# Optimization experiments

Measured on AMD Instinct MI355X. Metric: run time of the kernel, lower is better.

The kernel has to match this reference:

```python
import jax, jax.numpy as jnp
import numpy as np

EPS = 1e-5


def conv2d(x, w, b, pad, mode='reflect'):
    # x: [B,C,H,W], w: [O,I,kh,kw]
    if pad > 0:
        x = jnp.pad(x, ((0, 0), (0, 0), (pad, pad), (pad, pad)), mode=mode)
    y = jax.lax.conv_general_dilated(x, w, (1, 1), 'VALID',
                                     dimension_numbers=('NCHW', 'OIHW', 'NCHW'))
    return y + b[None, :, None, None]


def inorm(x):
    # InstanceNorm2d, no affine (nn.InstanceNorm2d default)
    m = jnp.mean(x, axis=(2, 3), keepdims=True)
    v = jnp.mean((x - m) ** 2, axis=(2, 3), keepdims=True)
    return (x - m) * jax.lax.rsqrt(v + EPS)


def upsample2(x):
    # nn.Upsample(scale_factor=2), default nearest
    return jnp.repeat(jnp.repeat(x, 2, axis=2), 2, axis=3)


def bilinear_sample(img, py, px):
    # img [B,C,H,W]; py/px [B,H,W] float coords; zero padding outside bounds
    B, C, H, W = img.shape
    y0 = jnp.floor(py)
    x0 = jnp.floor(px)
    wy1 = (py - y0)[:, None]
    wx1 = (px - x0)[:, None]
    wy0 = 1.0 - wy1
    wx0 = 1.0 - wx1
    y0i = y0.astype(jnp.int32)
    x0i = x0.astype(jnp.int32)
    flat = img.reshape(B, C, H * W)

    def tap(yi, xi):
        valid = (yi >= 0) & (yi < H) & (xi >= 0) & (xi < W)
        idx = jnp.clip(yi, 0, H - 1) * W + jnp.clip(xi, 0, W - 1)
        g = jnp.take_along_axis(flat, idx.reshape(B, 1, H * W), axis=2).reshape(B, C, H, W)
        return g * valid[:, None]

    return (tap(y0i, x0i) * wy0 * wx0 + tap(y0i, x0i + 1) * wy0 * wx1 +
            tap(y0i + 1, x0i) * wy1 * wx0 + tap(y0i + 1, x0i + 1) * wy1 * wx1)


def mdcn(x, offset, mask, w, b):
    # modulated deformable conv v2: 3x3, stride 1, pad 1, 1 deformable group
    # offset [B,18,H,W] read as interleaved (dy,dx) per kernel tap; mask [B,9,H,W]
    B, C, H, W = x.shape
    off = offset.reshape(B, 9, 2, H, W)
    base_y = jnp.arange(H, dtype=x.dtype)[None, :, None]
    base_x = jnp.arange(W, dtype=x.dtype)[None, None, :]
    cols = []
    for k in range(9):
        ky, kx = k // 3 - 1, k % 3 - 1
        py = base_y + ky + off[:, k, 0]
        px = base_x + kx + off[:, k, 1]
        cols.append(bilinear_sample(x, py, px) * mask[:, k][:, None])
    col = jnp.stack(cols, axis=2)  # [B,C,9,H,W]
    out = jnp.einsum('bckhw,ock->bohw', col, w.reshape(w.shape[0], C, 9))
    return out + b[None, :, None, None]


def dcn_block(out, skip, off_w, off_b, w, b):
    # ModulatedDeformConvPack(double=True): offsets from concat, deform conv on skip
    dc = jnp.concatenate([out, skip], axis=1)
    om = conv2d(dc, off_w, off_b, 1, mode='constant')
    o1, o2, m = jnp.split(om, 3, axis=1)
    offset = jnp.concatenate([o1, o2], axis=1)
    pre = mdcn(skip, offset, jax.nn.sigmoid(m), w, b)
    return jnp.concatenate([pre, out], axis=1), offset


def decoder_fwd(x, skip1, skip2,
                rb0_w1, rb0_b1, rb0_w2, rb0_b2,
                rb1_w1, rb1_b1, rb1_w2, rb1_b2,
                conv1_w, conv1_b, conv3_w, conv3_b,
                conv5_w, conv5_b, conv6_w, conv6_b,
                dcn2_off_w, dcn2_off_b, dcn2_w, dcn2_b,
                dcn1_off_w, dcn1_off_b, dcn1_w, dcn1_b):
    out = x
    # i=0: ResBlocks (2 resblocks, 'in' norm, relu, reflect pad)
    for (w1, b1, w2, b2) in ((rb0_w1, rb0_b1, rb0_w2, rb0_b2),
                             (rb1_w1, rb1_b1, rb1_w2, rb1_b2)):
        h = jax.nn.relu(inorm(conv2d(out, w1, b1, 1)))
        out = out + inorm(conv2d(h, w2, b2, 1))
    # i=1: Conv2dBlock(256->256, 5x5)
    out = jax.nn.relu(inorm(conv2d(out, conv1_w, conv1_b, 2)))
    # dcn_2 hook (baseline_idx=2 -> dcn_idx=[1,3])
    out, offset2 = dcn_block(out, skip2, dcn2_off_w, dcn2_off_b, dcn2_w, dcn2_b)
    # i=2: upsample
    out = upsample2(out)
    # i=3: Conv2dBlock(512->128, 5x5)
    out = jax.nn.relu(inorm(conv2d(out, conv3_w, conv3_b, 2)))
    # dcn hook
    out, offset1 = dcn_block(out, skip1, dcn1_off_w, dcn1_off_b, dcn1_w, dcn1_b)
    # i=4: upsample
    out = upsample2(out)
    # i=5: Conv2dBlock(256->64, 5x5)
    out = jax.nn.relu(inorm(conv2d(out, conv5_w, conv5_b, 2)))
    # i=6: Conv2dBlock(64->3, 7x7, no norm, tanh)
    out = jnp.tanh(conv2d(out, conv6_w, conv6_b, 3))
    offset_sum = 0.5 * (jnp.mean(jnp.abs(offset1)) + jnp.mean(jnp.abs(offset2)))
    return out, offset_sum


def setup_inputs() -> dict:
    key = jax.random.key(0)
    ks = iter(jax.random.split(key, 48))

    def randn(shape, scale=1.0):
        return jax.random.normal(next(ks), shape, dtype=jnp.float32) * scale

    def conv_w(o, i, k, scale=1.0):
        return randn((o, i, k, k), scale / float(np.sqrt(i * k * k)))

    d = {}
    d['x'] = randn((8, 256, 32, 32))
    d['skip1'] = randn((8, 128, 64, 64))
    d['skip2'] = randn((8, 256, 32, 32))
    for r in range(2):
        d[f'rb{r}_w1'] = conv_w(256, 256, 3)
        d[f'rb{r}_b1'] = randn((256,), 0.01)
        d[f'rb{r}_w2'] = conv_w(256, 256, 3)
        d[f'rb{r}_b2'] = randn((256,), 0.01)
    d['conv1_w'] = conv_w(256, 256, 5); d['conv1_b'] = randn((256,), 0.01)
    d['conv3_w'] = conv_w(128, 512, 5); d['conv3_b'] = randn((128,), 0.01)
    d['conv5_w'] = conv_w(64, 256, 5); d['conv5_b'] = randn((64,), 0.01)
    d['conv6_w'] = conv_w(3, 64, 7); d['conv6_b'] = randn((3,), 0.01)
    d['dcn2_off_w'] = conv_w(27, 512, 3, 0.1); d['dcn2_off_b'] = randn((27,), 0.01)
    d['dcn2_w'] = conv_w(256, 256, 3); d['dcn2_b'] = randn((256,), 0.01)
    d['dcn1_off_w'] = conv_w(27, 256, 3, 0.1); d['dcn1_off_b'] = randn((27,), 0.01)
    d['dcn1_w'] = conv_w(128, 128, 3); d['dcn1_b'] = randn((128,), 0.01)
    return d


def reference(x, skip1, skip2,
              rb0_w1, rb0_b1, rb0_w2, rb0_b2,
              rb1_w1, rb1_b1, rb1_w2, rb1_b2,
              conv1_w, conv1_b, conv3_w, conv3_b,
              conv5_w, conv5_b, conv6_w, conv6_b,
              dcn2_off_w, dcn2_off_b, dcn2_w, dcn2_b,
              dcn1_off_w, dcn1_off_b, dcn1_w, dcn1_b):
    return decoder_fwd(x, skip1, skip2,
                       rb0_w1, rb0_b1, rb0_w2, rb0_b2,
                       rb1_w1, rb1_b1, rb1_w2, rb1_b2,
                       conv1_w, conv1_b, conv3_w, conv3_b,
                       conv5_w, conv5_b, conv6_w, conv6_b,
                       dcn2_off_w, dcn2_off_b, dcn2_w, dcn2_b,
                       dcn1_off_w, dcn1_off_b, dcn1_w, dcn1_b)
```

## Files before the change

### kernel.cpp

```cpp
#include <hip/hip_runtime.h>
#include <hip/hip_bf16.h>
#include <math.h>

typedef __hip_bfloat16 bf16;
typedef unsigned short u16;
typedef __attribute__((ext_vector_type(8))) short short8;
typedef __attribute__((ext_vector_type(4))) float f32x4;

__device__ __forceinline__ float LD(const float* p) { return *p; }
__device__ __forceinline__ float LD(const bf16* p)  { return __bfloat162float(*p); }
__device__ __forceinline__ void  ST(float* p, float v) { *p = v; }
__device__ __forceinline__ void  ST(bf16* p, float v)  { *p = __float2bfloat16(v); }
__device__ __forceinline__ u16   f2b(float v) { bf16 h = __float2bfloat16(v); return *reinterpret_cast<u16*>(&h); }
__device__ __forceinline__ float b2fu(u16 u) { bf16 h = *reinterpret_cast<bf16*>(&u); return __bfloat162float(h); }

__global__ __launch_bounds__(256) void copy_kernel(const float* __restrict__ in,
                                                   float* __restrict__ out, int n) {
    int i = blockIdx.x * blockDim.x + threadIdx.x;
    if (i < n) out[i] = in[i];
}

__global__ __launch_bounds__(256) void nhwc_f32_kernel(const float* __restrict__ in,
                                                       float* __restrict__ out,
                                                       int C, int HW)
// ... 119 lines not shown
        int C1, int C,
        const u16* __restrict__ wth, const u16* __restrict__ wtl,
        const float* __restrict__ bias,
        void* __restrict__ outv, int O, int H, int W)
{
    constexpr int KK = K * K;
    constexpr int ATILE = NR * NCOL * 32;
    __shared__ __align__(16) u16 Ah[ATILE];
    __shared__ __align__(16) u16 Al[ASPLIT ? ATILE : 8];

    const int tid  = threadIdx.x;
    const int lane = tid & 63;
    const int wv   = tid >> 6;
    const int ln15 = lane & 15;
    const int quad = lane >> 4;
    const int mi = wv % MW, ni = wv / MW;
    int b, p0;
    if (XPIN) {
        const int flat = blockIdx.x + gridDim.x * blockIdx.y;
        b = flat & 7;
        p0 = (flat >> 3) * (MT * 16 * MW);
    } else {
        b = blockIdx.y;
        p0 = blockIdx.x * (MT * 16 * MW);
    }
    const int obase = blockIdx.z * 64;
    const int HW = H * W;
    const int SH = UP ? (H >> 1) : H;
    const int SW = UP ? (W >> 1) : W;
    const int SHW = SH * SW;
    const int PAD = K / 2;
    const int C2 = C - C1;
    const int nch = C >> 5;

    const int y0 = p0 / W;
    const int rbase = (y0 <= PAD) ? 0 : (UP ? ((y0 - PAD) >> 1) : (y0 - PAD));

    int rs[MT][K], cs[MT][K];
#pragma unroll
    for (int ms = 0; ms < MT; ++ms) {
        const int pm = p0 + mi * (MT * 16) + ms * 16 + ln15;
        const int ym = pm / W, xm = pm - ym * W;
#pragma unroll
        for (int tt = 0; tt < K; ++tt) {
            int yy = ym + tt - PAD;
            yy = yy < 0 ? -yy : yy; yy = yy >= H ? 2 * H - 2 - yy : yy;
            rs[ms][tt] = (UP ? (yy >> 1) : yy) - rbase;
            int xx = xm + tt - PAD;
            xx = xx < 0 ? -xx : xx; xx = xx >= W ? 2 * W - 2 - xx : xx;
            cs[ms][tt] = UP ? (xx >> 1) : xx;
        }
    }

    f32x4 acc[MT][2];
#pragma unroll
    for (int i = 0; i < MT; ++i)
#pragma unroll
        for (int j = 0; j < 2; ++j) acc[i][j] = (f32x4)0.f;

    for (int cc = 0; cc < nch; ++cc) {
        const int c0 = cc << 5;
        __syncthreads();
        for (int idx = tid; idx < NR * NCOL * 4; idx += MW * 128) {
            const int c_ = idx % NCOL;
            const int r_ = (idx / NCOL) % NR;
            const int cq = idx / (NCOL * NR);
            int rr = rbase + r_; rr = rr >= SH ? SH - 1 : rr;
            const int sidx = rr * SW + c_;
            short8 vh, vl;
#pragma unroll
            for (int q = 0; q < 8; ++q) {
                const int c = c0 + cq * 8 + q;
                float v;
                if (c < C1) v = LD(src1 + (size_t)(b * C1 + c) * SHW + sidx);
                else        v = LD(src2 + (size_t)(b * C2 + (c - C1)) * SHW + sidx);
                const u16 hv = f2b(v);
                vh[q] = (short)hv;
                if (ASPLIT) vl[q] = (short)f2b(v - b2fu(hv));
            }
            *(short8*)&Ah[idx * 8] = vh;
            if (ASPLIT) *(short8*)&Al[idx * 8] = vl;
        }
        __syncthreads();

#pragma unroll
        for (int t = 0; t < KK; ++t) {
            const int ty = t / K, tx = t - ty * K;
            const size_t wb0 = ((((size_t)t * nch + cc) * 4 + quad) * O
                                + obase + ni * 32 + ln15) * 8;
            const short8 b0h = *(const short8*)(wth + wb0);
            const short8 b1h = *(const short8*)(wth + wb0 + 128);
            const short8 b0l = *(const short8*)(wtl + wb0);
            const short8 b1l = *(const short8*)(wtl + wb0 + 128);
#pragma unroll
            for (int ms = 0; ms < MT; ++ms) {
                const int ao = ((quad * NR + rs[ms][ty]) * NCOL + cs[ms][tx]) * 8;
                const short8 a = *(const short8*)&Ah[ao];
                acc[ms][0] = __builtin_amdgcn_mfma_f32_16x16x32_bf16(a, b0h, acc[ms][0], 0, 0, 0);
                acc[ms][0] = __builtin_amdgcn_mfma_f32_16x16x32_bf16(a, b0l, acc[ms][0], 0, 0, 0);
                acc[ms][1] = __builtin_amdgcn_mfma_f32_16x16x32_bf16(a, b1h, acc[ms][1], 0, 0, 0);
                acc[ms][1] = __builtin_amdgcn_mfma_f32_16x16x32_bf16(a, b1l, acc[ms][1], 0, 0, 0);
                if (ASPLIT) {
                    const short8 al = *(const short8*)&Al[ao];
                    acc[ms][0] = __builtin_amdgcn_mfma_f32_16x16x32_bf16(al, b0h, acc[ms][0], 0, 0, 0);
                    acc[ms][1] = __builtin_amdgcn_mfma_f32_16x16x32_bf16(al, b1h, acc[ms][1], 0, 0, 0);
                }
            }
        }
    }

#pragma unroll
    for (int ms = 0; ms < MT; ++ms) {
#pragma unroll
        for (int ns = 0; ns < 2; ++ns) {
            const int o = obase + ni * 32 + ns * 16 + ln15;
            const float bv = (EPI == 3) ? (o < 3 ? bias[o] : 0.f) : bias[o];
            const f32x4 av = acc[ms][ns];
#pragma unroll
            for (int r = 0; r < 4; ++r) {
                const int pp = p0 + mi * (MT * 16) + ms * 16 + (quad << 2) + r;
                const float v = av[r] + bv;
                if (EPI == 0) {
                    ((float*)outv)[((size_t)(b * O + o)) * HW + pp] = v;
                } else if (EPI == 3) {
                    if (o < 3)
                        ((float*)outv)[((size_t)(b * 3 + o)) * HW + pp] = tanhf(v);
                } else {
                    ((bf16*)outv)[((size_t)(b * O + o)) * HW + pp] = __float2bfloat16(v);
                }
            }
        }
    }
}

template<typename T1, typename T2, int NR, int NCOL, int MT, int MW>
__global__ __launch_bounds__(MW * 128) void conv_mfma5(
        const T1* __restrict__ src1, const T2* __restrict__ src2,
        int C1, int C,
        const u16* __restrict__ wLh, const u16* __restrict__ wLl,
        const u16* __restrict__ wCh,
        const float* __restrict__ bias,
        bf16* __restrict__ out, int O, int H, int W)
{
    constexpr int NRR = NR + 1;
    __shared__ __align__(16) u16 Ah[4 * NRR * NCOL * 8];

    const int tid  = threadIdx.x;
    const int lane = tid & 63;
    const int wv   = tid >> 6;
    const int ln15 = lane & 15;
    const int quad = lane >> 4;
    const int mi = wv % MW, ni = wv / MW;
    const int b = blockIdx.y;
    const int p0 = blockIdx.x * (MT * 16 * MW);
    const int obase = blockIdx.z * 64;
    const int HW = H * W;
    const int SH = H >> 1, SW = W >> 1;
    const int SHW = SH * SW;
    const int C2 = C - C1;
    const int nch = C >> 5;
    const size_t U = (size_t)C * O;

    const int y0 = p0 / W;
    const int rbase = (y0 <= 2) ? 0 : ((y0 - 2) >> 1);

    const int ym0 = (p0 + mi * (MT * 16)) / W;
    const int ry = ym0 & 1;
    const int uu = ym0 >> 1;
    int r0 = uu - 1, r2 = uu + 1;
    r0 = r0 < 0 ? 1 : r0;
    r2 = r2 >= SH ? SH - 2 : r2;
    const int rg0 = r0 - rbase, rg1 = uu - rbase, rg2 = r2 - rbase;

    const bool isTopW = (ym0 <= 1), isBotW = (ym0 >= H - 2);
    const bool isBorderW = isTopW || isBotW;
    int cidx = 0;
    if (isTopW) cidx = (ym0 == 0) ? 1 : 0;
    if (isBotW) cidx = (ym0 == H - 2) ? 3 : 2;
    const bool blkTop = (p0 == 0);
    const bool blkBot = (p0 + MW * MT * 16 == HW);
    const bool blkEdge = blkTop || blkBot;

    int cs[MT][5];
#pragma unroll
    for (int ms = 0; ms < MT; ++ms) {
        const int pm = p0 + mi * (MT * 16) + ms * 16 + ln15;
        const int xm = pm % W;
#pragma unroll
        for (int tt = 0; tt < 5; ++tt) {
            int xx = xm + tt - 2;
            xx = xx < 0 ? -xx : xx; xx = xx >= W ? 2 * W - 2 - xx : xx;
            cs[ms][tt] = xx >> 1;
        }
    }

    f32x4 acc[MT][2];
#pragma unroll
    for (int i = 0; i < MT; ++i)
#pragma unroll
        for (int j = 0; j < 2; ++j) acc[i][j] = (f32x4)0.f;

    for (int cc = 0; cc < nch; ++cc) {
        const int c0 = cc << 5;
        __syncthreads();
        for (int idx = tid; idx < NR * NCOL * 4; idx += MW * 128) {
            const int c_ = idx % NCOL;
            const int r_ = (idx / NCOL) % NR;
            const int cq = idx / (NCOL * NR);
            int rr = rbase + r_; rr = rr >= SH ? SH - 1 : rr;
            const int sidx = rr * SW + c_;
            short8 vh;
#pragma unroll
            for (int q = 0; q < 8; ++q) {
                const int c = c0 + cq * 8 + q;
                float v;
                if (c < C1) v = LD(src1 + (size_t)(b * C1 + c) * SHW + sidx);
                else        v = LD(src2 + (size_t)(b * C2 + (c - C1)) * SHW + sidx);
                vh[q] = (short)f2b(v);
            }
            *(short8*)&Ah[((cq * NRR + r_) * NCOL + c_) * 8] = vh;
        }
        if (blkEdge) {
            const int ra = blkTop ? 0 : SH - 1;
            const int rb2 = blkTop ? 1 : SH - 2;
            for (int idx = tid; idx < NCOL * 4; idx += MW * 128) {
                const int c_ = idx % NCOL;
                const int cq = idx / NCOL;
                short8 vh;
#pragma unroll
                for (int q = 0; q < 8; ++q) {
                    const int c = c0 + cq * 8 + q;
                    float va, vb;
                    if (c < C1) {
                        const size_t base = (size_t)(b * C1 + c) * SHW;
                        va = LD(src1 + base + ra * SW + c_);
                        vb = LD(src1 + base + rb2 * SW + c_);
                    } else {
                        const size_t base = (size_t)(b * C2 + (c - C1)) * SHW;
                        va = LD(src2 + base + ra * SW + c_);
                        vb = LD(src2 + base + rb2 * SW + c_);
                    }
                    vh[q] = (short)f2b(va - vb);
                }
                *(short8*)&Ah[((cq * NRR + NR) * NCOL + c_) * 8] = vh;
            }
        }
        __syncthreads();

        const size_t wq = ((size_t)(cc * 4 + quad) * O + obase + ni * 32 + ln15) * 8;
#pragma unroll
        for (int j = 0; j < 3; ++j) {
            const int rgj = (j == 0) ? rg0 : (j == 1) ? rg1 : rg2;
#pragma unroll
            for (int tx = 0; tx < 5; ++tx) {
                const size_t wb = (size_t)((ry * 3 + j) * 5 + tx) * U + wq;
                const short8 b0h = *(const short8*)(wLh + wb);
                const short8 b1h = *(const short8*)(wLh + wb + 128);
                const short8 b0l = *(const short8*)(wLl + wb);
                const short8 b1l = *(const short8*)(wLl + wb + 128);
#pragma unroll
                for (int ms = 0; ms < MT; ++ms) {
                    const int ao = ((quad * NRR + rgj) * NCOL + cs[ms][tx]) * 8;
                    const short8 a = *(const short8*)&Ah[ao];
                    acc[ms][0] = __builtin_amdgcn_mfma_f32_16x16x32_bf16(a, b0h, acc[ms][0], 0, 0, 0);
                    acc[ms][0] = __builtin_amdgcn_mfma_f32_16x16x32_bf16(a, b0l, acc[ms][0], 0, 0, 0);
                    acc[ms][1] = __builtin_amdgcn_mfma_f32_16x16x32_bf16(a, b1h, acc[ms][1], 0, 0, 0);
                    acc[ms][1] = __builtin_amdgcn_mfma_f32_16x16x32_bf16(a, b1l, acc[ms][1], 0, 0, 0);
                }
            }
        }
        if (isBorderW) {
#pragma unroll
            for (int tx = 0; tx < 5; ++tx) {
                const size_t wb = (size_t)(cidx * 5 + tx) * U + wq;
                const short8 b0 = *(const short8*)(wCh + wb);
                const short8 b1 = *(const short8*)(wCh + wb + 128);
#pragma unroll
                for (int ms = 0; ms < MT; ++ms) {
                    const int ao = ((quad * NRR + NR) * NCOL + cs[ms][tx]) * 8;
                    const short8 a = *(const short8*)&Ah[ao];
                    acc[ms][0] = __builtin_amdgcn_mfma_f32_16x16x32_bf16(a, b0, acc[ms][0], 0, 0, 0);
                    acc[ms][1] = __builtin_amdgcn_mfma_f32_16x16x32_bf16(a, b1, acc[ms][1], 0, 0, 0);
                }
            }
        }
    }

#pragma unroll
    for (int ms = 0; ms < MT; ++ms) {
#pragma unroll
        for (int ns = 0; ns < 2; ++ns) {
            const int o = obase + ni * 32 + ns * 16 + ln15;
            const float bv = bias[o];
            const f32x4 av = acc[ms][ns];
#pragma unroll
            for (int r = 0; r < 4; ++r) {
                const int pp = p0 + mi * (MT * 16) + ms * 16 + (quad << 2) + r;
                out[((size_t)(b * O + o)) * HW + pp] = __float2bfloat16(av[r] + bv);
            }
        }
    }
}

template<typename OT, bool ASPLIT>
__global__ __launch_bounds__(256) void mdcn_mfma(
        const float* __restrict__ skipf,
        const float* __restrict__ om,
        const u16* __restrict__ wth, const u16* __restrict__ wtl,
        const float* __restrict__ bias,
        OT* __restrict__ out, int C, int O, int H, int W)
{
    __shared__ float tpy[576], tpxs[576], tms[576];
    __shared__ __align__(16) u16 Ah[2][2048];
    __shared__ __align__(16) u16 Al[ASPLIT ? 2 : 1][2048];
    __shared__ __align__(16) u16 Bs[2][2][2048];

    const int tid = threadIdx.x;
    const int lane = tid & 63;
    const int wv = tid >> 6;
    const int ln15 = lane & 15;
    const int quad = lane >> 4;
    const int mi = wv & 1, ni = wv >> 1;
    const int flat = blockIdx.x + gridDim.x * (blockIdx.y + 8 * blockIdx.z);
    const int b = flat & 7;
    const int rest = flat >> 3;
    const int p0 = (rest % gridDim.x) * 64;
    const int obase = (rest / gridDim.x) * 64;
    const int HW = H * W;
    const int nch = C >> 5;

    const float* omb = om + (size_t)b * 27 * HW;
    for (int i = tid; i < 576; i += 256) {
        const int k = i >> 6, px_ = i & 63;
        const int p = p0 + px_;
        const int y = p / W, x = p - y * W;
        const float dy = omb[(2 * k) * HW + p];
        const float dx = omb[(2 * k + 1) * HW + p];
        const float mk = 1.f / (1.f + expf(-omb[(18 + k) * HW + p]));
        float py = (float)(y + k / 3 - 1) + dy;
        float pxx = (float)(x + k % 3 - 1) + dx;
        py  = fminf(fmaxf(py, -2.f), (float)H + 1.f);
        pxx = fminf(fmaxf(pxx, -2.f), (float)W + 1.f);
        tpy[i] = py; tpxs[i] = pxx; tms[i] = mk;
    }
    __syncthreads();

    f32x4 acc[2][2];
#pragma unroll
    for (int i = 0; i < 2; ++i)
#pragma unroll
        for (int j = 0; j < 2; ++j) acc[i][j] = (f32x4)0.f;

    const float* xb = skipf + (size_t)b * HW * C;
    const int swA = (lane >> 1) & 3;
    const int awr = (lane * 4 + (wv ^ swA)) * 8;
    const int pix0 = mi * 32 + ln15;
    const int pix1 = pix0 + 16;
    const int ao0 = (pix0 * 4 + (quad ^ ((pix0 >> 1) & 3))) * 8;
    const int ao1 = (pix1 * 4 + (quad ^ ((pix1 >> 1) & 3))) * 8;
    const int bo0 = (quad * 64 + ni * 32 + ln15) * 8;
    const int bo1 = bo0 + 16 * 8;

    int chunk = 0;
    for (int k = 0; k < 9; ++k) {
        const float py = tpy[k * 64 + lane], pxx = tpxs[k * 64 + lane], mk = tms[k * 64 + lane];
        const float y0f = floorf(py), x0f = floorf(pxx);
        const int y0 = (int)y0f, x0 = (int)x0f;
        const float wy1 = py - y0f, wx1 = pxx - x0f;
        const float wy0 = 1.f - wy1, wx0 = 1.f - wx1;
        const bool r0v = (y0 >= 0 && y0 < H), r1v = (y0 + 1 >= 0 && y0 + 1 < H);
        const bool c0v = (x0 >= 0 && x0 < W), c1v = (x0 + 1 >= 0 && x0 + 1 < W);
        const float w00 = (r0v && c0v) ? wy0 * wx0 * mk : 0.f;
        const float w01 = (r0v && c1v) ? wy0 * wx1 * mk : 0.f;
        const float w10 = (r1v && c0v) ? wy1 * wx0 * mk : 0.f;
        const float w11 = (r1v && c1v) ? wy1 * wx1 * mk : 0.f;
        const int i00 = (r0v ? y0 : 0) * W + (c0v ? x0 : 0);
        const int i01 = (r0v ? y0 : 0) * W + (c1v ? x0 + 1 : 0);
        const int i10 = (r1v ? y0 + 1 : 0) * W + (c0v ? x0 : 0);
        const int i11 = (r1v ? y0 + 1 : 0) * W + (c1v ? x0 + 1 : 0);
        const float* pt00 = xb + (size_t)i00 * C;
        const float* pt01 = xb + (size_t)i01 * C;
        const float* pt10 = xb + (size_t)i10 * C;
        const float* pt11 = xb + (size_t)i11 * C;
        for (int cc = 0; cc < nch; ++cc, ++chunk) {
            const int s = chunk & 1;
            const int cbase = (cc << 5) + (wv << 3);
            {
                const f32x4 a00 = *(const f32x4*)(pt00 + cbase);
                const f32x4 b00 = *(const f32x4*)(pt00 + cbase + 4);
                const f32x4 a01 = *(const f32x4*)(pt01 + cbase);
                const f32x4 b01 = *(const f32x4*)(pt01 + cbase + 4);
                const f32x4 a10 = *(const f32x4*)(pt10 + cbase);
                const f32x4 b10 = *(const f32x4*)(pt10 + cbase + 4);
                const f32x4 a11 = *(const f32x4*)(pt11 + cbase);
                const f32x4 b11 = *(const f32x4*)(pt11 + cbase + 4);
                short8 vh, vl;
#pragma unroll
                for (int q = 0; q < 4; ++q) {
                    const float v = w00 * a00[q] + w01 * a01[q] + w10 * a10[q] + w11 * a11[q];
                    const u16 hv = f2b(v);
                    vh[q] = (short)hv;
                    if (ASPLIT) vl[q] = (short)f2b(v - b2fu(hv));
                }
#pragma unroll
                for (int q = 0; q < 4; ++q) {
                    const float v = w00 * b00[q] + w01 * b01[q] + w10 * b10[q] + w11 * b11[q];
                    const u16 hv = f2b(v);
                    vh[4 + q] = (short)hv;
                    if (ASPLIT) vl[4 + q] = (short)f2b(v - b2fu(hv));
                }
                *(short8*)&Ah[s][awr] = vh;
                if (ASPLIT) *(short8*)&Al[s][awr] = vl;
            }
            {
                const size_t base = ((((size_t)k * nch + cc) * 4 + wv) * O + obase + lane) * 8;
                *(short8*)&Bs[s][0][tid * 8] = *(const short8*)(wth + base);
                *(short8*)&Bs[s][1][tid * 8] = *(const short8*)(wtl + base);
            }
            __syncthreads();
            const short8 a0 = *(const short8*)&Ah[s][ao0];
            const short8 a1 = *(const short8*)&Ah[s][ao1];
            const short8 b0h = *(const short8*)&Bs[s][0][bo0];
            const short8 b1h = *(const short8*)&Bs[s][0][bo1];
            const short8 b0l = *(const short8*)&Bs[s][1][bo0];
            const short8 b1l = *(const short8*)&Bs[s][1][bo1];
            acc[0][0] = __builtin_amdgcn_mfma_f32_16x16x32_bf16(a0, b0h, acc[0][0], 0, 0, 0);
            acc[0][0] = __builtin_amdgcn_mfma_f32_16x16x32_bf16(a0, b0l, acc[0][0], 0, 0, 0);
            acc[0][1] = __builtin_amdgcn_mfma_f32_16x16x32_bf16(a0, b1h, acc[0][1], 0, 0, 0);
            acc[0][1] = __builtin_amdgcn_mfma_f32_16x16x32_bf16(a0, b1l, acc[0][1], 0, 0, 0);
            acc[1][0] = __builtin_amdgcn_mfma_f32_16x16x32_bf16(a1, b0h, acc[1][0], 0, 0, 0);
            acc[1][0] = __builtin_amdgcn_mfma_f32_16x16x32_bf16(a1, b0l, acc[1][0], 0, 0, 0);
            acc[1][1] = __builtin_amdgcn_mfma_f32_16x16x32_bf16(a1, b1h, acc[1][1], 0, 0, 0);
            acc[1][1] = __builtin_amdgcn_mfma_f32_16x16x32_bf16(a1, b1l, acc[1][1], 0, 0, 0);
            if (ASPLIT) {
                const short8 a0l = *(const short8*)&Al[s][ao0];
                const short8 a1l = *(const short8*)&Al[s][ao1];
                acc[0][0] = __builtin_amdgcn_mfma_f32_16x16x32_bf16(a0l, b0h, acc[0][0], 0, 0, 0);
                acc[0][1] = __builtin_amdgcn_mfma_f32_16x16x32_bf16(a0l, b1h, acc[0][1], 0, 0, 0);
                acc[1][0] = __builtin_amdgcn_mfma_f32_16x16x32_bf16(a1l, b0h, acc[1][0], 0, 0, 0);
                acc[1][1] = __builtin_amdgcn_mfma_f32_16x16x32_bf16(a1l, b1h, acc[1][1], 0, 0, 0);
            }
        }
    }

#pragma unroll
    for (int ms = 0; ms < 2; ++ms) {
#pragma unroll
        for (int ns = 0; ns < 2; ++ns) {
            const int o = obase + ni * 32 + ns * 16 + ln15;
            const float bv = bias[o];
#pragma unroll
            for (int r = 0; r < 4; ++r) {
                const int pp = p0 + mi * 32 + ms * 16 + (quad << 2) + r;
                ST(out + ((size_t)(b * O + o)) * HW + pp, acc[ms][ns][r] + bv);
            }
        }
    }
}

template<typename T1, typename T2, int K, bool REFLECT, bool UP, int NTN, int EPI, bool ASPLIT>
__global__ __launch_bounds__(256) void conv_mfma(
        const T1* __restrict__ src1, const T2* __restrict__ src2,
        int C1, int C,
        const u16* __restrict__ wth, const u16* __restrict__ wtl,
        const float* __restrict__ bias,
        void* __restrict__ outv, int O, int H, int W)
{
    constexpr int KK = K * K;
    __shared__ __align__(16) u16 As[64 * 40];
    __shared__ __align__(16) u16 Alo[ASPLIT ? 64 * 40 : 8];
    __shared__ __align__(16) u16 Bh[NTN * 16 * 40];
    __shared__ __align__(16) u16 Bl[NTN * 16 * 40];

    const int tid  = threadIdx.x;
    const int wv   = tid >> 6;
    const int lane = tid & 63;
    const int ln15 = lane & 15;
    const int flat = blockIdx.x + gridDim.x * blockIdx.y;
    const int b    = flat & 7;
    const int p0   = (flat >> 3) * 64;
    const int obase = blockIdx.z * (NTN * 16);
    const int HW = H * W;
    const int Hs = UP ? (H >> 1) : H;
    const int Ws = UP ? (W >> 1) : W;
    const int HsWs = Hs * Ws;
    const int PAD = K / 2;
    const int C2 = C - C1;
    const int m_stage = tid & 63;

    const int p = p0 + m_stage;
    const int y = p / W, x = p - y * W;
    int off[KK];
    float msk[KK];
#pragma unroll
    for (int ty = 0; ty < K; ++ty) {
#pragma unroll
        for (int tx = 0; tx < K; ++tx) {
            int yy = y + ty - PAD, xx = x + tx - PAD;
            bool vv = true;
            if (REFLECT) {
                yy = yy < 0 ? -yy : yy; yy = yy >= H ? 2 * H - 2 - yy : yy;
                xx = xx < 0 ? -xx : xx; xx = xx >= W ? 2 * W - 2 - xx : xx;
            } else {
                vv = (yy >= 0 && yy < H && xx >= 0 && xx < W);
                yy = yy < 0 ? 0 : (yy >= H ? H - 1 : yy);
                xx = xx < 0 ? 0 : (xx >= W ? W - 1 : xx);
            }
            off[ty * K + tx] = (UP ? (yy >> 1) : yy) * Ws + (UP ? (xx >> 1) : xx);
            msk[ty * K + tx] = vv ? 1.f : 0.f;
        }
    }

    f32x4 acc[NTN];
#pragma unroll
    for (int nt = 0; nt < NTN; ++nt) acc[nt] = (f32x4)0.f;

    const int aswz = (m_stage >> 3) & 3;
    const int awr  = m_stage * 40 + ((wv ^ aswz) << 3);
    const int arow = wv * 16 + ln15;
    const int ard  = arow * 40 + (((lane >> 4) ^ ((arow >> 3) & 3)) << 3);

    const int nch = C >> 5;
    for (int cc = 0; cc < nch; ++cc) {
        const int c0 = cc << 5;
        for (int t = 0; t < KK; ++t) {
            const int offt = off[t];
            const float mskt = msk[t];
            __syncthreads();
            {
                short8 avh, avl;
#pragma unroll
                for (int q = 0; q < 8; ++q) {
                    const int c = c0 + (wv << 3) + q;
                    float v;
                    if (c < C1) v = LD(src1 + ((size_t)(b * C1 + c)) * HsWs + offt);
                    else        v = LD(src2 + ((size_t)(b * C2 + (c - C1))) * HsWs + offt);
                    if (!REFLECT) v *= mskt;
                    const u16 hv = f2b(v);
                    avh[q] = (short)hv;
                    if (ASPLIT) avl[q] = (short)f2b(v - b2fu(hv));
                }
                *(short8*)&As[awr] = avh;
                if (ASPLIT) *(short8*)&Alo[awr] = avl;
            }
            for (int i = tid; i < NTN * 16 * 4; i += 256) {
                const int row = i >> 2, part = i & 3;
                int o = obase + row; if (o >= O) o = O - 1;
                const int pw = row * 40 + ((part ^ ((row >> 3) & 3)) << 3);
                const size_t wb = ((size_t)t * O + o) * C + c0 + (part << 3);
                *(short8*)&Bh[pw] = *(const short8*)(wth + wb);
                *(short8*)&Bl[pw] = *(const short8*)(wtl + wb);
            }
            __syncthreads();
            const short8 a = *(const short8*)&As[ard];
            short8 al;
            if (ASPLIT) al = *(const short8*)&Alo[ard];
#pragma unroll
            for (int nt = 0; nt < NTN; ++nt) {
                const int brow = nt * 16 + ln15;
                const int brd = brow * 40 + (((lane >> 4) ^ ((brow >> 3) & 3)) << 3);
                const short8 bh = *(const short8*)&Bh[brd];
                acc[nt] = __builtin_amdgcn_mfma_f32_16x16x32_bf16(a, bh, acc[nt], 0, 0, 0);
                const short8 bl = *(const short8*)&Bl[brd];
                acc[nt] = __builtin_amdgcn_mfma_f32_16x16x32_bf16(a, bl, acc[nt], 0, 0, 0);
                if (ASPLIT)
                    acc[nt] = __builtin_amdgcn_mfma_f32_16x16x32_bf16(al, bh, acc[nt], 0, 0, 0);
            }
        }
    }

#pragma unroll
    for (int nt = 0; nt < NTN; ++nt) {
        const int o = obase + nt * 16 + ln15;
        if (o < O) {
            const float bv = bias[o];
#pragma unroll
            for (int r = 0; r < 4; ++r) {
                const int pp = p0 + wv * 16 + ((lane >> 4) << 2) + r;
                const float v = acc[nt][r] + bv;
                const size_t oidx = ((size_t)(b * O + o)) * HW + pp;
                if (EPI == 0)      ((float*)outv)[oidx] = v;
                else if (EPI == 1) ((float*)outv)[oidx] = tanhf(v);
                else               ((bf16*)outv)[oidx] = __float2bfloat16(v);
            }
        }
    }
}

template<typename T>
__global__ __launch_bounds__(256) void inorm_kernel(T* __restrict__ buf,
                                                    float* __restrict__ resid,
                                                    int HW, int mode)
{
    __shared__ double sh0[256], sh1[256];
    const int pl = blockIdx.x;
    T* p = buf + (size_t)pl * HW;
    double s = 0.0, ss = 0.0;
    for (int i = threadIdx.x; i < HW; i += 256) {
        float v = LD(p + i);
        s += (double)v; ss += (double)v * (double)v;
    }
    sh0[threadIdx.x] = s; sh1[threadIdx.x] = ss;
    __syncthreads();
    for (int st = 128; st > 0; st >>= 1) {
        if (threadIdx.x < st) {
            sh0[threadIdx.x] += sh0[threadIdx.x + st];
            sh1[threadIdx.x] += sh1[threadIdx.x + st];
        }
        __syncthreads();
    }
    const double mean = sh0[0] / HW;
    const float m = (float)mean;
    const float var = (float)(sh1[0] / HW - mean * mean);
    const float inv = rsqrtf(var + 1e-5f);
    if (mode == 0) {
        for (int i = threadIdx.x; i < HW; i += 256) {
            float v = (LD(p + i) - m) * inv;
            ST(p + i, v > 0.f ? v : 0.f);
        }
    } else {
        float* r = resid + (size_t)pl * HW;
        for (int i = threadIdx.x; i < HW; i += 256)
            r[i] = r[i] + (LD(p + i) - m) * inv;
    }
}

__global__ void zero1_kernel(float* __restrict__ out) { if (threadIdx.x == 0) out[0] = 0.f; }

__global__ __launch_bounds__(256) void offsum_one(const float* __restrict__ om, int HW,
                                                  float* __restrict__ out)
{
    __shared__ double sh[256];
    const int n = 8 * 18 * HW;
    double s = 0.0;
    for (int i = blockIdx.x * 256 + threadIdx.x; i < n; i += gridDim.x * 256) {
        const int b = i / (18 * HW); const int r = i - b * 18 * HW;
        const int c = r / HW; const int p = r - c * HW;
        s += fabs((double)om[(size_t)(b * 27 + c) * HW + p]);
    }
    sh[threadIdx.x] = s;
    __syncthreads();
    for (int st = 128; st > 0; st >>= 1) {
        if (threadIdx.x < st) sh[threadIdx.x] += sh[threadIdx.x + st];
        __syncthreads();
    }
    if (threadIdx.x == 0) atomicAdd(out, (float)(0.5 * sh[0] / n));
}

extern "C" void kernel_launch(void* const* d_in, const int* in_sizes, int n_in,
                              void* d_out, int out_size, void* d_ws, size_t ws_size,
                              hipStream_t stream)
{
    if (n_in < 27) return;
    if (out_size < 393217) return;
    if (in_sizes[0] != 8 * 256 * 32 * 32) return;
    if (in_sizes[1] != 8 * 128 * 64 * 64) return;
    if (in_sizes[2] != 8 * 256 * 32 * 32) return;
    if (in_sizes[25] != 128 * 128 * 9) return;
    if (in_sizes[26] != 128) return;

    const float* x        = (const float*)d_in[0];
    const float* skip1    = (const float*)d_in[1];
    const float* skip2    = (const float*)d_in[2];
    const float* rbw[2][2] = {{(const float*)d_in[3], (const float*)d_in[5]},
                              {(const float*)d_in[7], (const float*)d_in[9]}};
    const float* rbb[2][2] = {{(const float*)d_in[4], (const float*)d_in[6]},
                              {(const float*)d_in[8], (const float*)d_in[10]}};
    const float* conv1_w = (const float*)d_in[11]; const float* conv1_b = (const float*)d_in[12];
    const float* conv3_w = (const float*)d_in[13]; const float* conv3_b = (const float*)d_in[14];
    const float* conv5_w = (const float*)d_in[15]; const float* conv5_b = (const float*)d_in[16];
    const float* conv6_w = (const float*)d_in[17]; const float* conv6_b = (const float*)d_in[18];
    const float* dcn2_off_w = (const float*)d_in[19]; const float* dcn2_off_b = (const float*)d_in[20];
    const float* dcn2_w = (const float*)d_in[21]; const float* dcn2_b = (const float*)d_in[22];
    const float* dcn1_off_w = (const float*)d_in[23]; const float* dcn1_off_b = (const float*)d_in[24];
    const float* dcn1_w = (const float*)d_in[25]; const float* dcn1_b = (const float*)d_in[26];

    float* outp = (float*)d_out;

    const size_t NEED_F32 = 9494528ull;
    if (ws_size < NEED_F32 * 4ull) return;

    float* ws = (float*)d_ws;
    const size_t NA = 2097152ull;
    float* A   = ws;
    float* Bb  = ws + NA;
    float* Tmp = ws + 2 * NA;
    float* om2 = ws + 3 * NA;
    float* om1 = om2 + 221184;
    bf16*  Fb  = (bf16*)(om1 + 884736);
    bf16*  Ib  = (bf16*)A;
    bf16*  Jb  = (bf16*)Bb;
    u16*   wm2h = (u16*)Tmp;
    u16*   wm2l = wm2h + 589824;
    u16*   wo2h = (u16*)(Tmp + 589824);
    u16*   wo2l = wo2h + 124416;
    u16*   wL3h = (u16*)Tmp;
    u16*   wL3l = wL3h + 30 * 65536;
    u16*   wC3h = wL3l + 30 * 65536;
    u16*   wm1h = (u16*)om2;
    u16*   wm1l = wm1h + 147456;
    u16*   wo1h = wm1h + 294912;
    u16*   wo1l = wo1h + 62208;
    u16*   wL5h = (u16*)om1;
    u16*   wL5l = wL5h + 30 * 16384;
    u16*   wC5h = wL5l + 30 * 16384;
    u16*   wt6h = (u16*)om2;
    u16*   wt6l = wt6h + 100352;
    u16*   wEh = (u16*)Fb;
    float* s2f = (float*)Fb;
    float* s1f = Bb;

    copy_kernel<<<8192, 256, 0, stream>>>(x, A, (int)NA);

    for (int r = 0; r < 2; ++r) {
        wsplit2_kernel<<<2304, 256, 0, stream>>>(rbw[r][0], wEh, wEh + 589824, 256, 256, 9);
        conv_mfma3<float, float, 3, false, 0, true, 4, 32, 2, 2, false><<<dim3(16, 8, 4), 256, 0, stream>>>(
            A, (const float*)nullptr, 256, 256, wEh, wEh + 589824, rbb[r][0], Bb, 256, 32, 32);
        inorm_kernel<float><<<2048, 256, 0, stream>>>(Bb, nullptr, 1024, 0);
        wsplit2_kernel<<<2304, 256, 0, stream>>>(rbw[r][1], wEh, wEh + 589824, 256, 256, 9);
        conv_mfma3<float, float, 3, false, 0, true, 4, 32, 2, 2, false><<<dim3(16, 8, 4), 256, 0, stream>>>(
            Bb, (const float*)nullptr, 256, 256, wEh, wEh + 589824, rbb[r][1], Tmp, 256, 32, 32);
        inorm_kernel<float><<<2048, 256, 0, stream>>>(Tmp, A, 1024, 1);
    }

    wsplit2_kernel<<<6400, 256, 0, stream>>>(conv1_w, wEh, wEh + 1638400, 256, 256, 25);
    conv_mfma3<float, float, 5, false, 0, true, 6, 32, 2, 2, false><<<dim3(16, 8, 4), 256, 0, stream>>>(
        A, (const float*)nullptr, 256, 256, wEh, wEh + 1638400, conv1_b, Bb, 256, 32, 32);
    inorm_kernel<float><<<2048, 256, 0, stream>>>(Bb, nullptr, 1024, 0);

    nhwc_f32_kernel<<<dim3(16, 8, 8), 256, 0, stream>>>(skip2, s2f, 256, 1024);

    wsplit_kernel<<<486, 256, 0, stream>>>(dcn2_off_w, wo2h, wo2l, 27, 512, 9);
    conv_mfma<float, float, 3, false, false, 2, 0, false><<<dim3(16, 8, 1), 256, 0, stream>>>(
        Bb, skip2, 256, 512, wo2h, wo2l, dcn2_off_b, om2, 27, 32, 32);
    wsplit2_kernel<<<2304, 256, 0, stream>>>(dcn2_w, wm2h, wm2l, 256, 256, 9);
    mdcn_mfma<float, true><<<dim3(16, 8, 4), 256, 0, stream>>>(
        s2f, om2, wm2h, wm2l, dcn2_b, A, 256, 256, 32, 32);

    zero1_kernel<<<1, 64, 0, stream>>>(outp + 393216);
    offsum_one<<<64, 256, 0, stream>>>(om2, 1024, outp + 393216);

    wsplitL_kernel<<<12800, 256, 0, stream>>>(conv3_w, wL3h, wL3l, wC3h, 128, 512);
    conv_mfma5<float, float, 4, 32, 4, 4><<<dim3(16, 8, 2), 512, 0, stream>>>(
        A, Bb, 256, 512, wL3h, wL3l, wC3h, conv3_b, Fb, 128, 64, 64);
    inorm_kernel<bf16><<<1024, 256, 0, stream>>>(Fb, nullptr, 4096, 0);

    wsplit_kernel<<<243, 256, 0, stream>>>(dcn1_off_w, wo1h, wo1l, 27, 256, 9);
    conv_mfma<bf16, float, 3, false, false, 2, 0, false><<<dim3(64, 8, 1), 256, 0, stream>>>(
        Fb, skip1, 128, 256, wo1h, wo1l, dcn1_off_b, om1, 27, 64, 64);
    wsplit2_kernel<<<576, 256, 0, stream>>>(dcn1_w, wm1h, wm1l, 128, 128, 9);
    nhwc_f32_kernel<<<dim3(64, 4, 8), 256, 0, stream>>>(skip1, s1f, 128, 4096);
    mdcn_mfma<bf16, true><<<dim3(64, 8, 2), 256, 0, stream>>>(
        s1f, om1, wm1h, wm1l, dcn1_b, Ib, 128, 128, 64, 64);

    offsum_one<<<64, 256, 0, stream>>>(om1, 4096, outp + 393216);

    wsplitL_kernel<<<3200, 256, 0, stream>>>(conv5_w, wL5h, wL5l, wC5h, 64, 256);
    conv_mfma5<bf16, bf16, 3, 64, 4, 4><<<dim3(64, 8, 1), 512, 0, stream>>>(
        Ib, Fb, 128, 256, wL5h, wL5l, wC5h, conv5_b, Jb, 64, 128, 128);
    inorm_kernel<bf16><<<512, 256, 0, stream>>>(Jb, nullptr, 16384, 0);

    wsplit2p_kernel<<<392, 256, 0, stream>>>(conv6_w, wt6h, wt6l, 3, 32, 64, 49);
    conv_mfma3<bf16, float, 7, false, 3, false, 10, 128, 4, 8, true><<<dim3(32, 8, 1), 1024, 0, stream>>>(
        Jb, (const float*)nullptr, 64, 64, wt6h, wt6l, conv6_b, (void*)outp, 32, 128, 128);
}
```

Baseline: 1.355 ms.

## Gather MDCN operands directly into MFMA register fragments, removing LDS staging

Measured after the change: 1.581 ms. 1.17x slower.

```diff
diff --git a/kernel.cpp b/kernel.cpp
--- a/kernel.cpp
+++ b/kernel.cpp
@@ -445,6 +445,54 @@
     }
 }
 
+__device__ __forceinline__ void bil_params(float py, float pxx, float mk, int H, int W,
+                                           float* w4, int* i4)
+{
+    const float y0f = floorf(py), x0f = floorf(pxx);
+    const int y0 = (int)y0f, x0 = (int)x0f;
+    const float wy1 = py - y0f, wx1 = pxx - x0f;
+    const float wy0 = 1.f - wy1, wx0 = 1.f - wx1;
+    const bool r0v = (y0 >= 0 && y0 < H), r1v = (y0 + 1 >= 0 && y0 + 1 < H);
+    const bool c0v = (x0 >= 0 && x0 < W), c1v = (x0 + 1 >= 0 && x0 + 1 < W);
+    w4[0] = (r0v && c0v) ? wy0 * wx0 * mk : 0.f;
+    w4[1] = (r0v && c1v) ? wy0 * wx1 * mk : 0.f;
+    w4[2] = (r1v && c0v) ? wy1 * wx0 * mk : 0.f;
+    w4[3] = (r1v && c1v) ? wy1 * wx1 * mk : 0.f;
+    i4[0] = (r0v ? y0 : 0) * W + (c0v ? x0 : 0);
+    i4[1] = (r0v ? y0 : 0) * W + (c1v ? x0 + 1 : 0);
+    i4[2] = (r1v ? y0 + 1 : 0) * W + (c0v ? x0 : 0);
+    i4[3] = (r1v ? y0 + 1 : 0) * W + (c1v ? x0 + 1 : 0);
+}
+
+template<bool ASPLIT>
+__device__ __forceinline__ void gather_frag(const float* __restrict__ xb, const float* w4,
+                                            const int* i4, int C, int cbase,
+                                            short8& vh, short8& vl)
+{
+    const float* p0 = xb + (size_t)i4[0] * C + cbase;
+    const float* p1 = xb + (size_t)i4[1] * C + cbase;
+    const float* p2 = xb + (size_t)i4[2] * C + cbase;
+    const float* p3 = xb + (size_t)i4[3] * C + cbase;
+    const f32x4 a0 = *(const f32x4*)p0, b0 = *(const f32x4*)(p0 + 4);
+    const f32x4 a1 = *(const f32x4*)p1, b1 = *(const f32x4*)(p1 + 4);
+    const f32x4 a2 = *(const f32x4*)p2, b2 = *(const f32x4*)(p2 + 4);
+    const f32x4 a3 = *(const f32x4*)p3, b3 = *(const f32x4*)(p3 + 4);
+#pragma unroll
+    for (int q = 0; q < 4; ++q) {
+        const float v = w4[0] * a0[q] + w4[1] * a1[q] + w4[2] * a2[q] + w4[3] * a3[q];
+        const u16 hv = f2b(v);
+        vh[q] = (short)hv;
+        if (ASPLIT) vl[q] = (short)f2b(v - b2fu(hv));
+    }
+#pragma unroll
+    for (int q = 0; q < 4; ++q) {
+        const float v = w4[0] * b0[q] + w4[1] * b1[q] + w4[2] * b2[q] + w4[3] * b3[q];
+        const u16 hv = f2b(v);
+        vh[4 + q] = (short)hv;
+        if (ASPLIT) vl[4 + q] = (short)f2b(v - b2fu(hv));
+    }
+}
+
 template<typename OT, bool ASPLIT>
 __global__ __launch_bounds__(256) void mdcn_mfma(
         const float* __restrict__ skipf,
@@ -454,9 +502,6 @@
         OT* __restrict__ out, int C, int O, int H, int W)
 {
     __shared__ float tpy[576], tpxs[576], tms[576];
-    __shared__ __align__(16) u16 Ah[2][2048];
-    __shared__ __align__(16) u16 Al[ASPLIT ? 2 : 1][2048];
-    __shared__ __align__(16) u16 Bs[2][2][2048];
 
     const int tid = threadIdx.x;
     const int lane = tid & 63;
@@ -495,89 +540,34 @@
         for (int j = 0; j < 2; ++j) acc[i][j] = (f32x4)0.f;
 
     const float* xb = skipf + (size_t)b * HW * C;
-    const int swA = (lane >> 1) & 3;
-    const int awr = (lane * 4 + (wv ^ swA)) * 8;
-    const int pix0 = mi * 32 + ln15;
-    const int pix1 = pix0 + 16;
-    const int ao0 = (pix0 * 4 + (quad ^ ((pix0 >> 1) & 3))) * 8;
-    const int ao1 = (pix1 * 4 + (quad ^ ((pix1 >> 1) & 3))) * 8;
-    const int bo0 = (quad * 64 + ni * 32 + ln15) * 8;
-    const int bo1 = bo0 + 16 * 8;
-
-    int chunk = 0;
+    const int pixA = mi * 32 + ln15;
+    const int pixB = pixA + 16;
+
     for (int k = 0; k < 9; ++k) {
-        const float py = tpy[k * 64 + lane], pxx = tpxs[k * 64 + lane], mk = tms[k * 64 + lane];
-        const float y0f = floorf(py), x0f = floorf(pxx);
-        const int y0 = (int)y0f, x0 = (int)x0f;
-        const float wy1 = py - y0f, wx1 = pxx - x0f;
-        const float wy0 = 1.f - wy1, wx0 = 1.f - wx1;
-        const bool r0v = (y0 >= 0 && y0 < H), r1v = (y0 + 1 >= 0 && y0 + 1 < H);
-        const bool c0v = (x0 >= 0 && x0 < W), c1v = (x0 + 1 >= 0 && x0 + 1 < W);
-        const float w00 = (r0v && c0v) ? wy0 * wx0 * mk : 0.f;
-        const float w01 = (r0v && c1v) ? wy0 * wx1 * mk : 0.f;
-        const float w10 = (r1v && c0v) ? wy1 * wx0 * mk : 0.f;
-        const float w11 = (r1v && c1v) ? wy1 * wx1 * mk : 0.f;
-        const int i00 = (r0v ? y0 : 0) * W + (c0v ? x0 : 0);
-        const int i01 = (r0v ? y0 : 0) * W + (c1v ? x0 + 1 : 0);
-        const int i10 = (r1v ? y0 + 1 : 0) * W + (c0v ? x0 : 0);
-        const int i11 = (r1v ? y0 + 1 : 0) * W + (c1v ? x0 + 1 : 0);
-        const float* pt00 = xb + (size_t)i00 * C;
-        const float* pt01 = xb + (size_t)i01 * C;
-        const float* pt10 = xb + (size_t)i10 * C;
-        const float* pt11 = xb + (size_t)i11 * C;
-        for (int cc = 0; cc < nch; ++cc, ++chunk) {
-            const int s = chunk & 1;
-            const int cbase = (cc << 5) + (wv << 3);
-            {
-                const f32x4 a00 = *(const f32x4*)(pt00 + cbase);
-                const f32x4 b00 = *(const f32x4*)(pt00 + cbase + 4);
-                const f32x4 a01 = *(const f32x4*)(pt01 + cbase);
-                const f32x4 b01 = *(const f32x4*)(pt01 + cbase + 4);
-                const f32x4 a10 = *(const f32x4*)(pt10 + cbase);
-                const f32x4 b10 = *(const f32x4*)(pt10 + cbase + 4);
-                const f32x4 a11 = *(const f32x4*)(pt11 + cbase);
-                const f32x4 b11 = *(const f32x4*)(pt11 + cbase + 4);
-                short8 vh, vl;
-#pragma unroll
-                for (int q = 0; q < 4; ++q) {
-                    const float v = w00 * a00[q] + w01 * a01[q] + w10 * a10[q] + w11 * a11[q];
-                    const u16 hv = f2b(v);
-                    vh[q] = (short)hv;
-                    if (ASPLIT) vl[q] = (short)f2b(v - b2fu(hv));
-                }
-#pragma unroll
-                for (int q = 0; q < 4; ++q) {
-                    const float v = w00 * b00[q] + w01 * b01[q] + w10 * b10[q] + w11 * b11[q];
-                    const u16 hv = f2b(v);
-                    vh[4 + q] = (short)hv;
-                    if (ASPLIT) vl[4 + q] = (short)f2b(v - b2fu(hv));
-                }
-                *(short8*)&Ah[s][awr] = vh;
-                if (ASPLIT) *(short8*)&Al[s][awr] = vl;
-            }
-            {
-                const size_t base = ((((size_t)k * nch + cc) * 4 + wv) * O + obase + lane) * 8;
-                *(short8*)&Bs[s][0][tid * 8] = *(const short8*)(wth + base);
-                *(short8*)&Bs[s][1][tid * 8] = *(const short8*)(wtl + base);
-            }
-            __syncthreads();
-            const short8 a0 = *(const short8*)&Ah[s][ao0];
-            const short8 a1 = *(const short8*)&Ah[s][ao1];
-            const short8 b0h = *(const short8*)&Bs[s][0][bo0];
-            const short8 b1h = *(const short8*)&Bs[s][0][bo1];
-            const short8 b0l = *(const short8*)&Bs[s][1][bo0];
-            const short8 b1l = *(const short8*)&Bs[s][1][bo1];
-            acc[0][0] = __builtin_amdgcn_mfma_f32_16x16x32_bf16(a0, b0h, acc[0][0], 0, 0, 0);
-            acc[0][0] = __builtin_amdgcn_mfma_f32_16x16x32_bf16(a0, b0l, acc[0][0], 0, 0, 0);
-            acc[0][1] = __builtin_amdgcn_mfma_f32_16x16x32_bf16(a0, b1h, acc[0][1], 0, 0, 0);
-            acc[0][1] = __builtin_amdgcn_mfma_f32_16x16x32_bf16(a0, b1l, acc[0][1], 0, 0, 0);
-            acc[1][0] = __builtin_amdgcn_mfma_f32_16x16x32_bf16(a1, b0h, acc[1][0], 0, 0, 0);
-            acc[1][0] = __builtin_amdgcn_mfma_f32_16x16x32_bf16(a1, b0l, acc[1][0], 0, 0, 0);
-            acc[1][1] = __builtin_amdgcn_mfma_f32_16x16x32_bf16(a1, b1h, acc[1][1], 0, 0, 0);
-            acc[1][1] = __builtin_amdgcn_mfma_f32_16x16x32_bf16(a1, b1l, acc[1][1], 0, 0, 0);
+        float wA[4], wB[4];
+        int iA[4], iB[4];
+        bil_params(tpy[k * 64 + pixA], tpxs[k * 64 + pixA], tms[k * 64 + pixA], H, W, wA, iA);
+        bil_params(tpy[k * 64 + pixB], tpxs[k * 64 + pixB], tms[k * 64 + pixB], H, W, wB, iB);
+        for (int cc = 0; cc < nch; ++cc) {
+            const int cbase = (cc << 5) + (quad << 3);
+            short8 a0h, a0l, a1h, a1l;
+            gather_frag<ASPLIT>(xb, wA, iA, C, cbase, a0h, a0l);
+            gather_frag<ASPLIT>(xb, wB, iB, C, cbase, a1h, a1l);
+            const size_t base = ((((size_t)k * nch + cc) * 4 + quad) * O
+                                 + obase + ni * 32 + ln15) * 8;
+            const short8 b0h = *(const short8*)(wth + base);
+            const short8 b1h = *(const short8*)(wth + base + 128);
+            const short8 b0l = *(const short8*)(wtl + base);
+            const short8 b1l = *(const short8*)(wtl + base + 128);
+            acc[0][0] = __builtin_amdgcn_mfma_f32_16x16x32_bf16(a0h, b0h, acc[0][0], 0, 0, 0);
+            acc[0][0] = __builtin_amdgcn_mfma_f32_16x16x32_bf16(a0h, b0l, acc[0][0], 0, 0, 0);
+            acc[0][1] = __builtin_amdgcn_mfma_f32_16x16x32_bf16(a0h, b1h, acc[0][1], 0, 0, 0);
+            acc[0][1] = __builtin_amdgcn_mfma_f32_16x16x32_bf16(a0h, b1l, acc[0][1], 0, 0, 0);
+            acc[1][0] = __builtin_amdgcn_mfma_f32_16x16x32_bf16(a1h, b0h, acc[1][0], 0, 0, 0);
+            acc[1][0] = __builtin_amdgcn_mfma_f32_16x16x32_bf16(a1h, b0l, acc[1][0], 0, 0, 0);
+            acc[1][1] = __builtin_amdgcn_mfma_f32_16x16x32_bf16(a1h, b1h, acc[1][1], 0, 0, 0);
+            acc[1][1] = __builtin_amdgcn_mfma_f32_16x16x32_bf16(a1h, b1l, acc[1][1], 0, 0, 0);
             if (ASPLIT) {
-                const short8 a0l = *(const short8*)&Al[s][ao0];
-                const short8 a1l = *(const short8*)&Al[s][ao1];
                 acc[0][0] = __builtin_amdgcn_mfma_f32_16x16x32_bf16(a0l, b0h, acc[0][0], 0, 0, 0);
                 acc[0][1] = __builtin_amdgcn_mfma_f32_16x16x32_bf16(a0l, b1h, acc[0][1], 0, 0, 0);
                 acc[1][0] = __builtin_amdgcn_mfma_f32_16x16x32_bf16(a1l, b0h, acc[1][0], 0, 0, 0);
```

## Compute two output-channel tiles per block in deformable conv, load weights directly

Applied to the files above, without the earlier changes.

New measurement: 1.303 ms. 1.04x faster.

```diff
diff --git a/kernel.cpp b/kernel.cpp
--- a/kernel.cpp
+++ b/kernel.cpp
@@ -445,7 +445,7 @@
     }
 }
 
-template<typename OT, bool ASPLIT>
+template<typename OT, bool ASPLIT, int OF>
 __global__ __launch_bounds__(256) void mdcn_mfma(
         const float* __restrict__ skipf,
         const float* __restrict__ om,
@@ -456,7 +456,6 @@
     __shared__ float tpy[576], tpxs[576], tms[576];
     __shared__ __align__(16) u16 Ah[2][2048];
     __shared__ __align__(16) u16 Al[ASPLIT ? 2 : 1][2048];
-    __shared__ __align__(16) u16 Bs[2][2][2048];
 
     const int tid = threadIdx.x;
     const int lane = tid & 63;
@@ -468,7 +467,7 @@
     const int b = flat & 7;
     const int rest = flat >> 3;
     const int p0 = (rest % gridDim.x) * 64;
-    const int obase = (rest / gridDim.x) * 64;
+    const int obase0 = (rest / gridDim.x) * (OF * 64);
     const int HW = H * W;
     const int nch = C >> 5;
 
@@ -488,11 +487,13 @@
     }
     __syncthreads();
 
-    f32x4 acc[2][2];
-#pragma unroll
-    for (int i = 0; i < 2; ++i)
-#pragma unroll
-        for (int j = 0; j < 2; ++j) acc[i][j] = (f32x4)0.f;
+    f32x4 acc[OF][2][2];
+#pragma unroll
+    for (int z = 0; z < OF; ++z)
+#pragma unroll
+        for (int i = 0; i < 2; ++i)
+#pragma unroll
+            for (int j = 0; j < 2; ++j) acc[z][i][j] = (f32x4)0.f;
 
     const float* xb = skipf + (size_t)b * HW * C;
     const int swA = (lane >> 1) & 3;
@@ -501,8 +502,6 @@
     const int pix1 = pix0 + 16;
     const int ao0 = (pix0 * 4 + (quad ^ ((pix0 >> 1) & 3))) * 8;
     const int ao1 = (pix1 * 4 + (quad ^ ((pix1 >> 1) & 3))) * 8;
-    const int bo0 = (quad * 64 + ni * 32 + ln15) * 8;
-    const int bo1 = bo0 + 16 * 8;
 
     int chunk = 0;
     for (int k = 0; k < 9; ++k) {
@@ -555,47 +554,53 @@
                 *(short8*)&Ah[s][awr] = vh;
                 if (ASPLIT) *(short8*)&Al[s][awr] = vl;
             }
-            {
-                const size_t base = ((((size_t)k * nch + cc) * 4 + wv) * O + obase + lane) * 8;
-                *(short8*)&Bs[s][0][tid * 8] = *(const short8*)(wth + base);
-                *(short8*)&Bs[s][1][tid * 8] = *(const short8*)(wtl + base);
-            }
             __syncthreads();
             const short8 a0 = *(const short8*)&Ah[s][ao0];
             const short8 a1 = *(const short8*)&Ah[s][ao1];
-            const short8 b0h = *(const short8*)&Bs[s][0][bo0];
-            const short8 b1h = *(const short8*)&Bs[s][0][bo1];
-            const short8 b0l = *(const short8*)&Bs[s][1][bo0];
-            const short8 b1l = *(const short8*)&Bs[s][1][bo1];
-            acc[0][0] = __builtin_amdgcn_mfma_f32_16x16x32_bf16(a0, b0h, acc[0][0], 0, 0, 0);
-            acc[0][0] = __builtin_amdgcn_mfma_f32_16x16x32_bf16(a0, b0l, acc[0][0], 0, 0, 0);
-            acc[0][1] = __builtin_amdgcn_mfma_f32_16x16x32_bf16(a0, b1h, acc[0][1], 0, 0, 0);
-            acc[0][1] = __builtin_amdgcn_mfma_f32_16x16x32_bf16(a0, b1l, acc[0][1], 0, 0, 0);
-            acc[1][0] = __builtin_amdgcn_mfma_f32_16x16x32_bf16(a1, b0h, acc[1][0], 0, 0, 0);
-            acc[1][0] = __builtin_amdgcn_mfma_f32_16x16x32_bf16(a1, b0l, acc[1][0], 0, 0, 0);
-            acc[1][1] = __builtin_amdgcn_mfma_f32_16x16x32_bf16(a1, b1h, acc[1][1], 0, 0, 0);
-            acc[1][1] = __builtin_amdgcn_mfma_f32_16x16x32_bf16(a1, b1l, acc[1][1], 0, 0, 0);
+            short8 a0l, a1l;
             if (ASPLIT) {
-                const short8 a0l = *(const short8*)&Al[s][ao0];
-                const short8 a1l = *(const short8*)&Al[s][ao1];
-                acc[0][0] = __builtin_amdgcn_mfma_f32_16x16x32_bf16(a0l, b0h, acc[0][0], 0, 0, 0);
-                acc[0][1] = __builtin_amdgcn_mfma_f32_16x16x32_bf16(a0l, b1h, acc[0][1], 0, 0, 0);
-                acc[1][0] = __builtin_amdgcn_mfma_f32_16x16x32_bf16(a1l, b0h, acc[1][0], 0, 0, 0);
-                acc[1][1] = __builtin_amdgcn_mfma_f32_16x16x32_bf16(a1l, b1h, acc[1][1], 0, 0, 0);
-            }
-        }
-    }
-
-#pragma unroll
-    for (int ms = 0; ms < 2; ++ms) {
-#pragma unroll
-        for (int ns = 0; ns < 2; ++ns) {
-            const int o = obase + ni * 32 + ns * 16 + ln15;
-            const float bv = bias[o];
-#pragma unroll
-            for (int r = 0; r < 4; ++r) {
-                const int pp = p0 + mi * 32 + ms * 16 + (quad << 2) + r;
-                ST(out + ((size_t)(b * O + o)) * HW + pp, acc[ms][ns][r] + bv);
+                a0l = *(const short8*)&Al[s][ao0];
+                a1l = *(const short8*)&Al[s][ao1];
+            }
+#pragma unroll
+            for (int zo = 0; zo < OF; ++zo) {
+                const size_t base = ((((size_t)k * nch + cc) * 4 + quad) * O
+                                     + obase0 + zo * 64 + ni * 32 + ln15) * 8;
+                const short8 b0h = *(const short8*)(wth + base);
+                const short8 b1h = *(const short8*)(wth + base + 128);
+                const short8 b0l = *(const short8*)(wtl + base);
+                const short8 b1l = *(const short8*)(wtl + base + 128);
+                acc[zo][0][0] = __builtin_amdgcn_mfma_f32_16x16x32_bf16(a0, b0h, acc[zo][0][0], 0, 0, 0);
+                acc[zo][0][0] = __builtin_amdgcn_mfma_f32_16x16x32_bf16(a0, b0l, acc[zo][0][0], 0, 0, 0);
+                acc[zo][0][1] = __builtin_amdgcn_mfma_f32_16x16x32_bf16(a0, b1h, acc[zo][0][1], 0, 0, 0);
+                acc[zo][0][1] = __builtin_amdgcn_mfma_f32_16x16x32_bf16(a0, b1l, acc[zo][0][1], 0, 0, 0);
+                acc[zo][1][0] = __builtin_amdgcn_mfma_f32_16x16x32_bf16(a1, b0h, acc[zo][1][0], 0, 0, 0);
+                acc[zo][1][0] = __builtin_amdgcn_mfma_f32_16x16x32_bf16(a1, b0l, acc[zo][1][0], 0, 0, 0);
+                acc[zo][1][1] = __builtin_amdgcn_mfma_f32_16x16x32_bf16(a1, b1h, acc[zo][1][1], 0, 0, 0);
+                acc[zo][1][1] = __builtin_amdgcn_mfma_f32_16x16x32_bf16(a1, b1l, acc[zo][1][1], 0, 0, 0);
+                if (ASPLIT) {
+                    acc[zo][0][0] = __builtin_amdgcn_mfma_f32_16x16x32_bf16(a0l, b0h, acc[zo][0][0], 0, 0, 0);
+                    acc[zo][0][1] = __builtin_amdgcn_mfma_f32_16x16x32_bf16(a0l, b1h, acc[zo][0][1], 0, 0, 0);
+                    acc[zo][1][0] = __builtin_amdgcn_mfma_f32_16x16x32_bf16(a1l, b0h, acc[zo][1][0], 0, 0, 0);
+                    acc[zo][1][1] = __builtin_amdgcn_mfma_f32_16x16x32_bf16(a1l, b1h, acc[zo][1][1], 0, 0, 0);
+                }
+            }
+        }
+    }
+
+#pragma unroll
+    for (int zo = 0; zo < OF; ++zo) {
+#pragma unroll
+        for (int ms = 0; ms < 2; ++ms) {
+#pragma unroll
+            for (int ns = 0; ns < 2; ++ns) {
+                const int o = obase0 + zo * 64 + ni * 32 + ns * 16 + ln15;
+                const float bv = bias[o];
+#pragma unroll
+                for (int r = 0; r < 4; ++r) {
+                    const int pp = p0 + mi * 32 + ms * 16 + (quad << 2) + r;
+                    ST(out + ((size_t)(b * O + o)) * HW + pp, acc[zo][ms][ns][r] + bv);
+                }
             }
         }
     }
@@ -877,7 +882,7 @@
     conv_mfma<float, float, 3, false, false, 2, 0, false><<<dim3(16, 8, 1), 256, 0, stream>>>(
         Bb, skip2, 256, 512, wo2h, wo2l, dcn2_off_b, om2, 27, 32, 32);
     wsplit2_kernel<<<2304, 256, 0, stream>>>(dcn2_w, wm2h, wm2l, 256, 256, 9);
-    mdcn_mfma<float, true><<<dim3(16, 8, 4), 256, 0, stream>>>(
+    mdcn_mfma<float, true, 2><<<dim3(16, 8, 2), 256, 0, stream>>>(
         s2f, om2, wm2h, wm2l, dcn2_b, A, 256, 256, 32, 32);
 
     zero1_kernel<<<1, 64, 0, stream>>>(outp + 393216);
@@ -893,7 +898,7 @@
         Fb, skip1, 128, 256, wo1h, wo1l, dcn1_off_b, om1, 27, 64, 64);
     wsplit2_kernel<<<576, 256, 0, stream>>>(dcn1_w, wm1h, wm1l, 128, 128, 9);
     nhwc_f32_kernel<<<dim3(64, 4, 8), 256, 0, stream>>>(skip1, s1f, 128, 4096);
-    mdcn_mfma<bf16, true><<<dim3(64, 8, 2), 256, 0, stream>>>(
+    mdcn_mfma<bf16, true, 2><<<dim3(64, 8, 1), 256, 0, stream>>>(
         s1f, om1, wm1h, wm1l, dcn1_b, Ib, 128, 128, 64, 64);
 
     offsum_one<<<64, 256, 0, stream>>>(om1, 4096, outp + 393216);
```
